# Optimization experiments

Hardware: AMD Instinct MI355X
Metric: run time of the kernel (lower is better)

Reference implementation:

```python
import jax, jax.numpy as jnp
import numpy as np

DIM = 512
CTX_DIM = 512
NUM_HEADS = 8
DIM_HEAD = 64
INNER = NUM_HEADS * DIM_HEAD  # 512
B, N, CTX_LEN = 4, 2048, 2048


def setup_inputs() -> dict:
    key = jax.random.key(0)
    ks = jax.random.split(key, 6)
    x = jax.random.normal(ks[0], (B, DIM, N), dtype=jnp.float32)
    context = jax.random.normal(ks[1], (B, CTX_DIM, CTX_LEN), dtype=jnp.float32)
    # Linear weights stored as (in, out); bias only on output projection.
    W_q = jax.random.normal(ks[2], (DIM, INNER), dtype=jnp.float32) / np.sqrt(DIM)
    W_kv = jax.random.normal(ks[3], (CTX_DIM, 2 * INNER), dtype=jnp.float32) / np.sqrt(CTX_DIM)
    W_out = jax.random.normal(ks[4], (INNER, DIM), dtype=jnp.float32) / np.sqrt(INNER)
    b_out = jax.random.normal(ks[5], (DIM,), dtype=jnp.float32) * 0.01
    return {"x": x, "context": context, "W_q": W_q, "W_kv": W_kv,
            "W_out": W_out, "b_out": b_out}


def reference(x, context, W_q, W_kv, W_out, b_out):
    scale = DIM_HEAD ** -0.5
    xs = jnp.swapaxes(x, 1, 2)        # (b, n, dim)
    cs = jnp.swapaxes(context, 1, 2)  # (b, ctx_len, ctx_dim)
    b, n, _ = xs.shape
    m = cs.shape[1]
    q = xs @ W_q                       # (b, n, inner)
    kv = cs @ W_kv                     # (b, m, 2*inner)
    k, v = jnp.split(kv, 2, axis=-1)
    # split heads -> (b, h, len, d)
    q = q.reshape(b, n, NUM_HEADS, DIM_HEAD).transpose(0, 2, 1, 3)
    k = k.reshape(b, m, NUM_HEADS, DIM_HEAD).transpose(0, 2, 1, 3)
    v = v.reshape(b, m, NUM_HEADS, DIM_HEAD).transpose(0, 2, 1, 3)
    attn = jnp.einsum('bhqd,bhkd->bhqk', q * scale, k)
    attn = jax.nn.softmax(attn, axis=-1)
    out = jnp.einsum('bhqk,bhkd->bhqd', attn, v)
    out = out.transpose(0, 2, 1, 3).reshape(b, n, INNER)
    out = out @ W_out + b_out          # (b, n, dim); dropout p=0 is identity
    return jnp.swapaxes(out, 1, 2)     # (b, dim, n)
```

## Files before the change

### kernel.cpp

```cpp
#include <hip/hip_runtime.h>
#include <hip/hip_bf16.h>

typedef __attribute__((ext_vector_type(8))) short bf16x8;
typedef __attribute__((ext_vector_type(4))) float f32x4;
typedef __attribute__((ext_vector_type(16))) float f32x16;
typedef __attribute__((ext_vector_type(8))) unsigned short ushort8v;
typedef __attribute__((ext_vector_type(4))) unsigned short ushort4v;

#define MFMA16(a, b, c) __builtin_amdgcn_mfma_f32_16x16x32_bf16((a), (b), (c), 0, 0, 0)
#define MFMA32(a, b, c) __builtin_amdgcn_mfma_f32_32x32x16_bf16((a), (b), (c), 0, 0, 0)

__device__ __forceinline__ unsigned int cvtpk(float a, float b) {
  unsigned int r;
  asm("v_cvt_pk_bf16_f32 %0, %1, %2" : "=v"(r) : "v"(a), "v"(b));
  return r;
}
__device__ __forceinline__ unsigned short f2bf(float f) {
  return (unsigned short)cvtpk(f, f);
}

__global__ __launch_bounds__(256) void transpose_all_kernel(
    const float* __restrict__ x, const float* __restrict__ ctx,
    const float* __restrict__ Wq, const float* __restrict__ Wkv,
    const float* __restrict__ Wo, unsigned short* __restrict__ xt,
    unsigned short* __restrict__ ct, unsigned short* __restrict__ Wqt,
    unsigned short* __restrict__ Wkvt, unsigned short* __restrict__ Wot) {
  __shared__ float tile[64][33];
  int z = blockIdx.z;
  const float* in;
  unsigned short* out;
  int C;
  if (z < 4)      { in = x + (size_t)z * 512 * 2048;         out = xt + (size_t)z * 2048 * 512;        C = 2048; }
  else if (z < 8) { in = ctx + (size_t)(z - 4) * 512 * 2048; out = ct + (size_t)(z - 4) * 2048 * 512;  C = 2048; }
  else if (z == 8) { in = Wq;  out = Wqt;  C = 512; }
  else if (z == 9) { in = Wkv; out = Wkvt; C = 1024; }
  else             { in = Wo;  out = Wot;  C = 512; }
  int c0 = blockIdx.x * 32;
  if (c0 >= C) return;
  int r0 = blockIdx.y * 64;
  int tid = threadIdx.x, cl = tid & 31, rl = tid >> 5;
#pragma unroll
  for (int k = 0; k < 8; ++k)
    tile[rl + 8 * k][cl] = in[(size_t)(r0 + rl + 8 * k) * C + c0 + cl];
  __syncthreads();
  int c = tid >> 3, rc = (tid & 7) * 8;
  union { unsigned int wd[4]; ushort8v v; } p;
#pragma unroll
  for (int jj = 0; jj < 4; ++jj)
    p.wd[jj] = cvtpk(tile[rc + 2 * jj][c], tile[rc + 2 * jj + 1][c]);
  *(ushort8v*)&out[(size_t)(c0 + c) * 512 + r0 + rc] = p.v;
}

__device__ __forceinline__ void gemm_acc128(
    const unsigned short* __restrict__ A, const unsigned short* __restrict__ Bt,
    int l0, int o0, f32x4 acc[4][4],
    unsigned short* As, unsigned short* Bs) {
  int tid = threadIdx.x, lane = tid & 63, wv = tid >> 6;
  int wl = wv >> 1, wo = wv & 1, lg = lane >> 4, lr = lane & 15;
  int r8 = lane >> 3, gc = (lane & 7) ^ r8;
  const unsigned short* ga = A + (size_t)(l0 + wv * 32 + r8) * 512 + gc * 8;
  const unsigned short* gb = Bt + (size_t)(o0 + wv * 32 + r8) * 512 + gc * 8;
  int rowbA[4], rswA[4], rowbB[4], rswB[4];
#pragma unroll
  for (int f = 0; f < 4; ++f) {
    int r = wl * 64 + f * 16 + lr;
    rowbA[f] = (r >> 3) * 1040 + (r & 7) * 128;
    rswA[f] = (r & 7) << 4;
    int rb = wo * 64 + f * 16 + lr;
    rowbB[f] = (rb >> 3) * 1040 + (rb & 7) * 128;
    rswB[f] = (rb & 7) << 4;
  }
  const char* aC = (const char*)As;
  const char* bC = (const char*)Bs;
  for (int kb = 0; kb < 512; kb += 64) {
#pragma unroll
    for (int j = 0; j < 4; ++j) {
      __builtin_amdgcn_global_load_lds(
          (const __attribute__((address_space(1))) void*)(ga + (size_t)(j * 8) * 512 + kb),
          (__attribute__((address_space(3))) void*)(As + (wv * 4 + j) * 520), 16, 0, 0);
      __builtin_amdgcn_global_load_lds(
          (const __attribute__((address_space(1))) void*)(gb + (size_t)(j * 8) * 512 + kb),
          (__attribute__((address_space(3))) void*)(Bs + (wv * 4 + j) * 520), 16, 0, 0);
    }
    __syncthreads();
#pragma unroll
    for (int kc = 0; kc < 2; ++kc) {
      bf16x8 af[4], bfr[4];
#pragma unroll
      for (int mf = 0; mf < 4; ++mf)
        af[mf] = *(const bf16x8*)(aC + rowbA[mf] + (((4 * kc + lg) << 4) ^ rswA[mf]));
#pragma unroll
      for (int nf = 0; nf < 4; ++nf)
        bfr[nf] = *(const bf16x8*)(bC + rowbB[nf] + (((4 * kc + lg) << 4) ^ rswB[nf]));
#pragma unroll
      for (int mf = 0; mf < 4; ++mf)
#pragma unroll
        for (int nf = 0; nf < 4; ++nf)
          acc[mf][nf] = MFMA16(af[mf], bfr[nf], acc[mf][nf]);
    }
    __syncthreads();
  }
}

__global__ __launch_bounds__(256) void gemm_qkv_kernel(
    const unsigned short* __restrict__ xt, const unsigned short* __restrict__ ct,
    const unsigned short* __restrict__ Wqt, const unsigned short* __restrict__ Wkvt,
    unsigned short* __restrict__ Qb, unsigned short* __restrict__ K,
    unsigned short* __restrict__ Vt) {
  __shared__ unsigned short As[8320];
  __shared__ unsigned short Bs[8320];
  f32x4 acc[4][4] = {};
  int l0 = blockIdx.x * 128;
  int yy = blockIdx.y;
  const unsigned short* A;
  const unsigned short* Bt;
  int o0;
  if (yy < 4) { A = xt; Bt = Wqt; o0 = yy * 128; }
  else        { A = ct; Bt = Wkvt; o0 = (yy - 4) * 128; }
  gemm_acc128(A, Bt, l0, o0, acc, As, Bs);
  int lane = threadIdx.x & 63, wave = threadIdx.x >> 6;
  int wl = wave >> 1, wo = wave & 1, lg = lane >> 4, lr = lane & 15;
  if (yy < 4) {
    const float qs = 0.18033688011112042f;
#pragma unroll
    for (int mf = 0; mf < 4; ++mf)
#pragma unroll
      for (int nf = 0; nf < 4; ++nf)
#pragma unroll
        for (int r = 0; r < 4; ++r) {
          int row = l0 + wl * 64 + mf * 16 + 4 * lg + r;
          int col = o0 + wo * 64 + nf * 16 + lr;
          Qb[(size_t)row * 512 + col] = f2bf(acc[mf][nf][r] * qs);
        }
  } else if (o0 < 512) {
#pragma unroll
    for (int mf = 0; mf < 4; ++mf)
#pragma unroll
      for (int nf = 0; nf < 4; ++nf)
#pragma unroll
        for (int r = 0; r < 4; ++r) {
          int row = l0 + wl * 64 + mf * 16 + 4 * lg + r;
          int col = o0 + wo * 64 + nf * 16 + lr;
          K[(size_t)row * 512 + col] = f2bf(acc[mf][nf][r]);
        }
  } else {
    int b = l0 >> 11;
#pragma unroll
    for (int mf = 0; mf < 4; ++mf)
#pragma unroll
      for (int nf = 0; nf < 4; ++nf) {
        int m0v = (l0 & 2047) + wl * 64 + mf * 16 + 4 * lg;
        int msw = (m0v & ~12) | ((m0v & 4) << 1) | ((m0v & 8) >> 1);
        int oh = (o0 - 512) + wo * 64 + nf * 16 + lr;
        int h = oh >> 6, d = oh & 63;
        ushort4v pk;
#pragma unroll
        for (int r = 0; r < 4; ++r) pk[r] = f2bf(acc[mf][nf][r]);
        *(ushort4v*)&Vt[(size_t)((b * 8 + h) * 64 + d) * 2048 + msw] = pk;
      }
  }
}

__global__ __launch_bounds__(256) void gemm_out_kernel(
    const unsigned short* __restrict__ A, const unsigned short* __restrict__ Bt,
    float* __restrict__ Out, const float* __restrict__ bias) {
  __shared__ unsigned short As[8320];
  __shared__ unsigned short Bs[8320];
  f32x4 acc[4][4] = {};
  int l0 = blockIdx.x * 128, o0 = blockIdx.y * 128;
  gemm_acc128(A, Bt, l0, o0, acc, As, Bs);
  int lane = threadIdx.x & 63, wave = threadIdx.x >> 6;
  int wl = wave >> 1, wo = wave & 1, lg = lane >> 4, lr = lane & 15;
#pragma unroll
  for (int mf = 0; mf < 4; ++mf)
#pragma unroll
    for (int nf = 0; nf < 4; ++nf) {
      int row = l0 + wl * 64 + mf * 16 + 4 * lg;
      int col = o0 + wo * 64 + nf * 16 + lr;
      int b = row >> 11, n = row & 2047;
      float bv = bias[col];
      f32x4 v = acc[mf][nf];
#pragma unroll
      for (int r = 0; r < 4; ++r) v[r] += bv;
      *(f32x4*)&Out[((size_t)(b * 512 + col)) * 2048 + n] = v;
    }
}

__global__ __launch_bounds__(128, 2) void attn_kernel(
    const unsigned short* __restrict__ Qb, const unsigned short* __restrict__ Kb,
    const unsigned short* __restrict__ Vt, unsigned short* __restrict__ Ob) {
  __shared__ unsigned short Ksh[2][4160];
  __shared__ unsigned short Vsh[2][4160];
  int id = blockIdx.x;
  int slot = id & 7, qb = (id >> 3) & 31, hbhi = id >> 8;
  int hb = hbhi * 8 + slot;
  int h = hb & 7, b = hb >> 3;
  int tid = threadIdx.x, w = tid >> 6, lane = tid & 63;
  int l31 = lane & 31, hi = lane >> 5;
  int qrow = b * 2048 + qb * 64 + w * 32 + l31;

  const unsigned short* qp = Qb + (size_t)qrow * 512 + h * 64 + 8 * hi;
  bf16x8 qf[4];
#pragma unroll
  for (int dk = 0; dk < 4; ++dk) qf[dk] = *(const bf16x8*)(qp + 16 * dk);

  int r8 = lane >> 3, gc = (lane & 7) ^ r8;
  const unsigned short* kg =
      Kb + (size_t)(b * 2048 + w * 32 + r8) * 512 + h * 64 + gc * 8;
  const unsigned short* vg =
      Vt + (size_t)((b * 8 + h) * 64 + w * 32 + r8) * 2048 + gc * 8;
  int grp0 = w * 4;

#define STAGE(t, bi)                                                               \
  {                                                                                \
    _Pragma("unroll") for (int j2 = 0; j2 < 4; ++j2) {                             \
      __builtin_amdgcn_global_load_lds(                                            \
          (const __attribute__((address_space(1))) void*)(kg +                     \
              (size_t)((t) * 64 + j2 * 8) * 512),                                  \
          (__attribute__((address_space(3))) void*)(&Ksh[bi][(grp0 + j2) * 520]),  \
          16, 0, 0);                                                               \
      __builtin_amdgcn_global_load_lds(                                            \
          (const __attribute__((address_space(1))) void*)(vg +                     \
              (size_t)(j2 * 8) * 2048 + (t) * 64),                                 \
          (__attribute__((address_space(3))) void*)(&Vsh[bi][(grp0 + j2) * 520]),  \
          16, 0, 0);                                                               \
    }                                                                              \
  }

  STAGE(0, 0);
  STAGE(1, 1);

  int rowoff0 = (l31 >> 3) * 1040 + (l31 & 7) * 128;
  int rowoff1 = rowoff0 + 4 * 1040;
  int swz = (l31 & 7) << 4;

  f32x16 o0 = {}, o1 = {};
  float lsum = 0.0f;

#pragma unroll 1
  for (int t = 0; t < 32; ++t) {
    int bi = t & 1;
    if (t == 31) { asm volatile("s_waitcnt vmcnt(0)" ::: "memory"); }
    else         { asm volatile("s_waitcnt vmcnt(8)" ::: "memory"); }
    __builtin_amdgcn_sched_barrier(0);
    __builtin_amdgcn_s_barrier();
    __builtin_amdgcn_sched_barrier(0);

    const char* kbC = (const char*)&Ksh[bi][0];
    const char* vbC = (const char*)&Vsh[bi][0];
    bf16x8 kfr[8];
#pragma unroll
    for (int dk = 0; dk < 4; ++dk) {
      kfr[dk] = *(const bf16x8*)(kbC + rowoff0 + (((2 * dk + hi) << 4) ^ swz));
      kfr[4 + dk] = *(const bf16x8*)(kbC + rowoff1 + (((2 * dk + hi) << 4) ^ swz));
    }
    bf16x8 vfa[4], vfb[4];
#pragma unroll
    for (int q = 0; q < 4; ++q) {
      vfa[q] = *(const bf16x8*)(vbC + rowoff0 + (((2 * q + hi) << 4) ^ swz));
      vfb[q] = *(const bf16x8*)(vbC + rowoff1 + (((2 * q + hi) << 4) ^ swz));
    }
    asm volatile("s_waitcnt lgkmcnt(0)" ::: "memory");
    __builtin_amdgcn_sched_barrier(0);
    __builtin_amdgcn_s_barrier();
    __builtin_amdgcn_sched_barrier(0);
    if (t < 30) STAGE(t + 2, bi);

    __builtin_amdgcn_s_setprio(1);
    f32x16 sA = {}, sB = {};
#pragma unroll
    for (int dk = 0; dk < 4; ++dk) {
      sA = MFMA32(kfr[dk], qf[dk], sA);
      sB = MFMA32(kfr[4 + dk], qf[dk], sB);
    }
    __builtin_amdgcn_s_setprio(0);

#pragma unroll
    for (int i = 0; i < 16; ++i) {
      sA[i] = __builtin_amdgcn_exp2f(sA[i]);
      sB[i] = __builtin_amdgcn_exp2f(sB[i]);
    }
    float u[8];
#pragma unroll
    for (int i = 0; i < 8; ++i) u[i] = (sA[i] + sA[i + 8]) + (sB[i] + sB[i + 8]);
    lsum += ((u[0] + u[1]) + (u[2] + u[3])) + ((u[4] + u[5]) + (u[6] + u[7]));

    bf16x8 ptA[2], ptB[2];
    {
      union { unsigned int wd[4]; bf16x8 v; } uu;
      uu.wd[0] = cvtpk(sA[0], sA[1]); uu.wd[1] = cvtpk(sA[2], sA[3]);
      uu.wd[2] = cvtpk(sA[4], sA[5]); uu.wd[3] = cvtpk(sA[6], sA[7]);
      ptA[0] = uu.v;
      uu.wd[0] = cvtpk(sA[8], sA[9]); uu.wd[1] = cvtpk(sA[10], sA[11]);
      uu.wd[2] = cvtpk(sA[12], sA[13]); uu.wd[3] = cvtpk(sA[14], sA[15]);
      ptA[1] = uu.v;
      uu.wd[0] = cvtpk(sB[0], sB[1]); uu.wd[1] = cvtpk(sB[2], sB[3]);
      uu.wd[2] = cvtpk(sB[4], sB[5]); uu.wd[3] = cvtpk(sB[6], sB[7]);
      ptB[0] = uu.v;
      uu.wd[0] = cvtpk(sB[8], sB[9]); uu.wd[1] = cvtpk(sB[10], sB[11]);
      uu.wd[2] = cvtpk(sB[12], sB[13]); uu.wd[3] = cvtpk(sB[14], sB[15]);
      ptB[1] = uu.v;
    }

    __builtin_amdgcn_s_setprio(1);
    o0 = MFMA32(vfa[0], ptA[0], o0);
    o0 = MFMA32(vfa[1], ptA[1], o0);
    o1 = MFMA32(vfb[0], ptA[0], o1);
    o1 = MFMA32(vfb[1], ptA[1], o1);
    o0 = MFMA32(vfa[2], ptB[0], o0);
    o0 = MFMA32(vfa[3], ptB[1], o0);
    o1 = MFMA32(vfb[2], ptB[0], o1);
    o1 = MFMA32(vfb[3], ptB[1], o1);
    __builtin_amdgcn_s_setprio(0);
  }
#undef STAGE

  float ltot = lsum + __shfl_xor(lsum, 32, 64);
  float rinv = 1.0f / ltot;
  unsigned short* ob = Ob + (size_t)qrow * 512 + h * 64 + 4 * hi;
#pragma unroll
  for (int i = 0; i < 8; ++i) {
    int dvlo = ((2 * i) & 3) + 8 * ((2 * i) >> 2);
    *(unsigned int*)(ob + dvlo) = cvtpk(o0[2 * i] * rinv, o0[2 * i + 1] * rinv);
    *(unsigned int*)(ob + 32 + dvlo) = cvtpk(o1[2 * i] * rinv, o1[2 * i + 1] * rinv);
  }
}

extern "C" void kernel_launch(void* const* d_in, const int* in_sizes, int n_in,
                              void* d_out, int out_size, void* d_ws, size_t ws_size,
                              hipStream_t stream) {
  const float* x   = (const float*)d_in[0];
  const float* ctx = (const float*)d_in[1];
  const float* Wq  = (const float*)d_in[2];
  const float* Wkv = (const float*)d_in[3];
  const float* Wo  = (const float*)d_in[4];
  const float* bo  = (const float*)d_in[5];
  float* out = (float*)d_out;

  char* ws = (char*)d_ws;
  unsigned short* xt   = (unsigned short*)(ws + 0);
  unsigned short* ct   = (unsigned short*)(ws + 8388608);
  unsigned short* Wqt  = (unsigned short*)(ws + 16777216);
  unsigned short* Wkvt = (unsigned short*)(ws + 17301504);
  unsigned short* Wot  = (unsigned short*)(ws + 18350080);
  unsigned short* Qb   = (unsigned short*)(ws + 18874368);
  unsigned short* Kb   = (unsigned short*)(ws + 27262976);
  unsigned short* Vtb  = (unsigned short*)(ws + 35651584);
  unsigned short* Ob   = (unsigned short*)(ws + 44040192);

  transpose_all_kernel<<<dim3(64, 8, 11), 256, 0, stream>>>(
      x, ctx, Wq, Wkv, Wo, xt, ct, Wqt, Wkvt, Wot);

  gemm_qkv_kernel<<<dim3(64, 12), 256, 0, stream>>>(xt, ct, Wqt, Wkvt, Qb, Kb, Vtb);

  attn_kernel<<<dim3(1024), 128, 0, stream>>>(Qb, Kb, Vtb, Ob);

  gemm_out_kernel<<<dim3(64, 4), 256, 0, stream>>>(Ob, Wot, out, bo);
}
```

Before: 96.91 us.

## Split attention key tiles across two wave pairs and merge partial outputs

The attention block grows from 2 to 4 waves. Each pair of waves takes half of every 64-key tile and accumulates its own partial P·V and row sum. The two halves are then combined through shared memory before normalising and writing out. This halves the MFMA and exp work per wave and doubles the waves available to hide latency, at the cost of an extra LDS reduction, more barriers, and higher register and occupancy pressure from the launch bounds of 256 threads with 4 blocks.

```diff
diff --git a/kernel.cpp b/kernel.cpp
--- a/kernel.cpp
+++ b/kernel.cpp
@@ -186,7 +186,7 @@
     }
 }
 
-__global__ __launch_bounds__(128, 2) void attn_kernel(
+__global__ __launch_bounds__(256, 4) void attn_kernel(
     const unsigned short* __restrict__ Qb, const unsigned short* __restrict__ Kb,
     const unsigned short* __restrict__ Vt, unsigned short* __restrict__ Ob) {
   __shared__ unsigned short Ksh[2][4160];
@@ -196,8 +196,9 @@
   int hb = hbhi * 8 + slot;
   int h = hb & 7, b = hb >> 3;
   int tid = threadIdx.x, w = tid >> 6, lane = tid & 63;
+  int qg = w & 1, kh = w >> 1;
   int l31 = lane & 31, hi = lane >> 5;
-  int qrow = b * 2048 + qb * 64 + w * 32 + l31;
+  int qrow = b * 2048 + qb * 64 + qg * 32 + l31;
 
   const unsigned short* qp = Qb + (size_t)qrow * 512 + h * 64 + 8 * hi;
   bf16x8 qf[4];
@@ -206,14 +207,14 @@
 
   int r8 = lane >> 3, gc = (lane & 7) ^ r8;
   const unsigned short* kg =
-      Kb + (size_t)(b * 2048 + w * 32 + r8) * 512 + h * 64 + gc * 8;
+      Kb + (size_t)(b * 2048 + w * 16 + r8) * 512 + h * 64 + gc * 8;
   const unsigned short* vg =
-      Vt + (size_t)((b * 8 + h) * 64 + w * 32 + r8) * 2048 + gc * 8;
-  int grp0 = w * 4;
+      Vt + (size_t)((b * 8 + h) * 64 + w * 16 + r8) * 2048 + gc * 8;
+  int grp0 = w * 2;
 
 #define STAGE(t, bi)                                                               \
   {                                                                                \
-    _Pragma("unroll") for (int j2 = 0; j2 < 4; ++j2) {                             \
+    _Pragma("unroll") for (int j2 = 0; j2 < 2; ++j2) {                             \
       __builtin_amdgcn_global_load_lds(                                            \
           (const __attribute__((address_space(1))) void*)(kg +                     \
               (size_t)((t) * 64 + j2 * 8) * 512),                                  \
@@ -230,6 +231,8 @@
   STAGE(0, 0);
   STAGE(1, 1);
 
+  int rowK = kh * 32 + l31;
+  int rowoffK = (rowK >> 3) * 1040 + (rowK & 7) * 128;
   int rowoff0 = (l31 >> 3) * 1040 + (l31 & 7) * 128;
   int rowoff1 = rowoff0 + 4 * 1040;
   int swz = (l31 & 7) << 4;
@@ -241,24 +244,23 @@
   for (int t = 0; t < 32; ++t) {
     int bi = t & 1;
     if (t == 31) { asm volatile("s_waitcnt vmcnt(0)" ::: "memory"); }
-    else         { asm volatile("s_waitcnt vmcnt(8)" ::: "memory"); }
+    else         { asm volatile("s_waitcnt vmcnt(4)" ::: "memory"); }
     __builtin_amdgcn_sched_barrier(0);
     __builtin_amdgcn_s_barrier();
     __builtin_amdgcn_sched_barrier(0);
 
     const char* kbC = (const char*)&Ksh[bi][0];
     const char* vbC = (const char*)&Vsh[bi][0];
-    bf16x8 kfr[8];
-#pragma unroll
-    for (int dk = 0; dk < 4; ++dk) {
-      kfr[dk] = *(const bf16x8*)(kbC + rowoff0 + (((2 * dk + hi) << 4) ^ swz));
-      kfr[4 + dk] = *(const bf16x8*)(kbC + rowoff1 + (((2 * dk + hi) << 4) ^ swz));
-    }
-    bf16x8 vfa[4], vfb[4];
-#pragma unroll
-    for (int q = 0; q < 4; ++q) {
-      vfa[q] = *(const bf16x8*)(vbC + rowoff0 + (((2 * q + hi) << 4) ^ swz));
-      vfb[q] = *(const bf16x8*)(vbC + rowoff1 + (((2 * q + hi) << 4) ^ swz));
+    bf16x8 kfr[4];
+#pragma unroll
+    for (int dk = 0; dk < 4; ++dk)
+      kfr[dk] = *(const bf16x8*)(kbC + rowoffK + (((2 * dk + hi) << 4) ^ swz));
+    bf16x8 vfa[2], vfb[2];
+#pragma unroll
+    for (int qq = 0; qq < 2; ++qq) {
+      int ch = (2 * (2 * kh + qq) + hi) << 4;
+      vfa[qq] = *(const bf16x8*)(vbC + rowoff0 + (ch ^ swz));
+      vfb[qq] = *(const bf16x8*)(vbC + rowoff1 + (ch ^ swz));
     }
     asm volatile("s_waitcnt lgkmcnt(0)" ::: "memory");
     __builtin_amdgcn_sched_barrier(0);
@@ -267,62 +269,64 @@
     if (t < 30) STAGE(t + 2, bi);
 
     __builtin_amdgcn_s_setprio(1);
-    f32x16 sA = {}, sB = {};
-#pragma unroll
-    for (int dk = 0; dk < 4; ++dk) {
-      sA = MFMA32(kfr[dk], qf[dk], sA);
-      sB = MFMA32(kfr[4 + dk], qf[dk], sB);
-    }
+    f32x16 sA = {};
+#pragma unroll
+    for (int dk = 0; dk < 4; ++dk) sA = MFMA32(kfr[dk], qf[dk], sA);
     __builtin_amdgcn_s_setprio(0);
 
 #pragma unroll
-    for (int i = 0; i < 16; ++i) {
-      sA[i] = __builtin_amdgcn_exp2f(sA[i]);
-      sB[i] = __builtin_amdgcn_exp2f(sB[i]);
-    }
+    for (int i = 0; i < 16; ++i) sA[i] = __builtin_amdgcn_exp2f(sA[i]);
     float u[8];
 #pragma unroll
-    for (int i = 0; i < 8; ++i) u[i] = (sA[i] + sA[i + 8]) + (sB[i] + sB[i + 8]);
+    for (int i = 0; i < 8; ++i) u[i] = sA[i] + sA[i + 8];
     lsum += ((u[0] + u[1]) + (u[2] + u[3])) + ((u[4] + u[5]) + (u[6] + u[7]));
 
-    bf16x8 ptA[2], ptB[2];
+    bf16x8 pt[2];
     {
       union { unsigned int wd[4]; bf16x8 v; } uu;
       uu.wd[0] = cvtpk(sA[0], sA[1]); uu.wd[1] = cvtpk(sA[2], sA[3]);
       uu.wd[2] = cvtpk(sA[4], sA[5]); uu.wd[3] = cvtpk(sA[6], sA[7]);
-      ptA[0] = uu.v;
+      pt[0] = uu.v;
       uu.wd[0] = cvtpk(sA[8], sA[9]); uu.wd[1] = cvtpk(sA[10], sA[11]);
       uu.wd[2] = cvtpk(sA[12], sA[13]); uu.wd[3] = cvtpk(sA[14], sA[15]);
-      ptA[1] = uu.v;
-      uu.wd[0] = cvtpk(sB[0], sB[1]); uu.wd[1] = cvtpk(sB[2], sB[3]);
-      uu.wd[2] = cvtpk(sB[4], sB[5]); uu.wd[3] = cvtpk(sB[6], sB[7]);
-      ptB[0] = uu.v;
-      uu.wd[0] = cvtpk(sB[8], sB[9]); uu.wd[1] = cvtpk(sB[10], sB[11]);
-      uu.wd[2] = cvtpk(sB[12], sB[13]); uu.wd[3] = cvtpk(sB[14], sB[15]);
-      ptB[1] = uu.v;
+      pt[1] = uu.v;
     }
 
     __builtin_amdgcn_s_setprio(1);
-    o0 = MFMA32(vfa[0], ptA[0], o0);
-    o0 = MFMA32(vfa[1], ptA[1], o0);
-    o1 = MFMA32(vfb[0], ptA[0], o1);
-    o1 = MFMA32(vfb[1], ptA[1], o1);
-    o0 = MFMA32(vfa[2], ptB[0], o0);
-    o0 = MFMA32(vfa[3], ptB[1], o0);
-    o1 = MFMA32(vfb[2], ptB[0], o1);
-    o1 = MFMA32(vfb[3], ptB[1], o1);
+    o0 = MFMA32(vfa[0], pt[0], o0);
+    o0 = MFMA32(vfa[1], pt[1], o0);
+    o1 = MFMA32(vfb[0], pt[0], o1);
+    o1 = MFMA32(vfb[1], pt[1], o1);
     __builtin_amdgcn_s_setprio(0);
   }
 #undef STAGE
 
-  float ltot = lsum + __shfl_xor(lsum, 32, 64);
-  float rinv = 1.0f / ltot;
-  unsigned short* ob = Ob + (size_t)qrow * 512 + h * 64 + 4 * hi;
-#pragma unroll
-  for (int i = 0; i < 8; ++i) {
-    int dvlo = ((2 * i) & 3) + 8 * ((2 * i) >> 2);
-    *(unsigned int*)(ob + dvlo) = cvtpk(o0[2 * i] * rinv, o0[2 * i + 1] * rinv);
-    *(unsigned int*)(ob + 32 + dvlo) = cvtpk(o1[2 * i] * rinv, o1[2 * i + 1] * rinv);
+  float lt = lsum + __shfl_xor(lsum, 32, 64);
+  __syncthreads();
+  float* mo = (float*)&Ksh[0][0];
+  float* mlp = (float*)&Vsh[0][0];
+  if (kh == 1) {
+    float* d = mo + (qg * 64 + lane) * 32;
+#pragma unroll
+    for (int i = 0; i < 16; ++i) { d[i] = o0[i]; d[16 + i] = o1[i]; }
+    mlp[qg * 64 + lane] = lt;
+  }
+  __syncthreads();
+  if (kh == 0) {
+    const float* d = mo + (qg * 64 + lane) * 32;
+    float ltot = lt + mlp[qg * 64 + lane];
+    float rinv = 1.0f / ltot;
+    unsigned short* ob = Ob + (size_t)qrow * 512 + h * 64 + 4 * hi;
+#pragma unroll
+    for (int i = 0; i < 8; ++i) {
+      int dvlo = ((2 * i) & 3) + 8 * ((2 * i) >> 2);
+      float a0 = (o0[2 * i] + d[2 * i]) * rinv;
+      float a1 = (o0[2 * i + 1] + d[2 * i + 1]) * rinv;
+      *(unsigned int*)(ob + dvlo) = cvtpk(a0, a1);
+      float b0v = (o1[2 * i] + d[16 + 2 * i]) * rinv;
+      float b1v = (o1[2 * i + 1] + d[16 + 2 * i + 1]) * rinv;
+      *(unsigned int*)(ob + 32 + dvlo) = cvtpk(b0v, b1v);
+    }
   }
 }
 
@@ -353,7 +357,7 @@
 
   gemm_qkv_kernel<<<dim3(64, 12), 256, 0, stream>>>(xt, ct, Wqt, Wkvt, Qb, Kb, Vtb);
 
-  attn_kernel<<<dim3(1024), 128, 0, stream>>>(Qb, Kb, Vtb, Ob);
+  attn_kernel<<<dim3(1024), 256, 0, stream>>>(Qb, Kb, Vtb, Ob);
 
   gemm_out_kernel<<<dim3(64, 4), 256, 0, stream>>>(Ob, Wot, out, bo);
 }
```

Result: no change. 97.81 us (+0.9%).
